# Optimization experiments

Hardware: AMD Instinct MI355X
Metric: run time of the kernel (lower is better)

## Reference

```python
import jax, jax.numpy as jnp
import numpy as np

SLICES = [(12, 1), (13, 1)]  # (input_width, hidden_size=1) per slice


def _lstm_last_hidden(xs, W_ih, W_hh, b):
    """Run a standard (PyTorch gate order i,f,g,o) LSTM over time, return last h.
    xs: [T, B, in]; W_ih: [4*H, in]; W_hh: [4*H, H]; b: [4*H] (b_ih + b_hh).
    Returns h_T: [B, H].
    """
    B = xs.shape[1]
    H = W_hh.shape[1]
    h0 = jnp.zeros((B, H), xs.dtype)
    c0 = jnp.zeros((B, H), xs.dtype)

    def step(carry, xt):
        h, c = carry
        gates = xt @ W_ih.T + h @ W_hh.T + b  # [B, 4H]
        i, f, g, o = jnp.split(gates, 4, axis=-1)
        i = jax.nn.sigmoid(i)
        f = jax.nn.sigmoid(f)
        g = jnp.tanh(g)
        o = jax.nn.sigmoid(o)
        c = f * c + i * g
        h = o * jnp.tanh(c)
        return (h, c), None

    (hT, _), _ = jax.lax.scan(step, (h0, c0), xs)
    return hT


def setup_inputs() -> dict:
    key = jax.random.key(0)
    ks = jax.random.split(key, 9)
    B, T, F = 4096, 512, 25
    nb_out = 1
    s = 0.1
    x = jax.random.normal(ks[0], (B, T, F), dtype=jnp.float32)
    # slice-1 LSTM (input 12, hidden 1)
    W_ih1 = jax.random.normal(ks[1], (4, 12), dtype=jnp.float32) * s
    W_hh1 = jax.random.normal(ks[2], (4, 1), dtype=jnp.float32) * s
    b1 = jax.random.normal(ks[3], (4,), dtype=jnp.float32) * s
    # slice-2 LSTM (input 13, hidden 1)
    W_ih2 = jax.random.normal(ks[4], (4, 13), dtype=jnp.float32) * s
    W_hh2 = jax.random.normal(ks[5], (4, 1), dtype=jnp.float32) * s
    b2 = jax.random.normal(ks[6], (4,), dtype=jnp.float32) * s
    # output head Linear(2, nb_out)
    W_out = jax.random.normal(ks[7], (nb_out, 2), dtype=jnp.float32) * s
    b_out = jax.random.normal(ks[8], (nb_out,), dtype=jnp.float32) * s
    return {"x": x, "W_ih1": W_ih1, "W_hh1": W_hh1, "b1": b1,
            "W_ih2": W_ih2, "W_hh2": W_hh2, "b2": b2,
            "W_out": W_out, "b_out": b_out}


def reference(x, W_ih1, W_hh1, b1, W_ih2, W_hh2, b2, W_out, b_out):
    # x: [B, T, 25] -> time-major [T, B, 25]
    xs = jnp.transpose(x, (1, 0, 2))
    h1 = _lstm_last_hidden(xs[..., :12], W_ih1, W_hh1, b1)   # [B, 1]
    h2 = _lstm_last_hidden(xs[..., 12:], W_ih2, W_hh2, b2)   # [B, 1]
    h = jnp.concatenate([h1, h2], axis=-1)                   # [B, 2] == lstm_out[:, -1, :]
    out = h @ W_out.T + b_out                                # [B, nb_out]
    return jax.nn.sigmoid(out)
```

## Files before the change

### kernel.cpp

```cpp
#include <hip/hip_runtime.h>
#include <stdint.h>


#define T_STEPS 512
#define F_IN    25
#define TC      16
#define NTILES  (T_STEPS / TC)
#define CH      8
#define XROW    520
#define ZROW    (TC * 8 + 8)
#define LOG2E   1.44269504088896340736f

typedef const __attribute__((address_space(1))) void* as1_cvp;
typedef __attribute__((address_space(3)))       void* as3_vp;

__device__ __forceinline__ void gll16(const float* gsrc, const float* ldst) {
  __builtin_amdgcn_global_load_lds((as1_cvp)(uintptr_t)gsrc,
                                   (as3_vp)(uint32_t)(uintptr_t)ldst, 16, 0, 0);
}

__device__ __forceinline__ float sigm(float v) {
  return __builtin_amdgcn_rcpf(1.0f + __builtin_amdgcn_exp2f(v * (-LOG2E)));
}
__device__ __forceinline__ float tanh_(float v) {
  return fmaf(2.0f, __builtin_amdgcn_rcpf(1.0f + __builtin_amdgcn_exp2f(v * (-2.0f * LOG2E))), -1.0f);
}

__device__ __forceinline__ void prefetch_tile(const float* __restrict__ x, int b0, int tile,
                                              float* xbuf, int lane) {
  const float* base = x + (size_t)b0 * (T_STEPS * F_IN) + tile * (TC * F_IN);
  const int i1 = lane * 4;
  int i2 = 256 + lane * 4;
  if (i2 > 396) i2 = 396;
#pragma unroll
  for (int cc = 0; cc < CH; ++cc) {
    const float* g0 = base + cc * (T_STEPS * F_IN);
    gll16(g0 + i1, xbuf + cc * XROW);
    gll16(g0 + i2, xbuf + cc * XROW + 256);
  }
}

__device__ __forceinline__ void gemv_tile(const float* __restrict__ xbuf, float* __restrict__ zbuf,
                                          int c, int lt,
                                          const float* __restrict__ w1, const float* __restrict__ w2,
                                          const float* __restrict__ zb) {
#pragma unroll
  for (int p = 0; p < 2; ++p) {
    const int tl = p * 8 + lt;
    const float* xr = xbuf + c * XROW + tl * F_IN;
    float z[8];
#pragma unroll
    for (int j = 0; j < 8; ++j) z[j] = zb[j];
#pragma unroll
    for (int f = 0; f < 12; ++f) {
      const float xv = xr[f];
#pragma unroll
      for (int j = 0; j < 4; ++j) z[j] = fmaf(w1[j * 12 + f], xv, z[j]);
    }
#pragma unroll
    for (int f = 0; f < 13; ++f) {
      const float xv = xr[12 + f];
#pragma unroll
      for (int j = 0; j < 4; ++j) z[4 + j] = fmaf(w2[j * 13 + f], xv, z[4 + j]);
    }
    float4* zp = (float4*)(zbuf + c * ZROW + tl * 8);
    zp[0] = make_float4(z[0], z[1], z[2], z[3]);
    zp[1] = make_float4(z[4], z[5], z[6], z[7]);
  }
}

__device__ __forceinline__ void scan_tile(const float* __restrict__ zbuf, int c, int zoff,
                                          const float* __restrict__ whh, float& hv, float& cv) {
#pragma unroll
  for (int t = 0; t < TC; ++t) {
    const float4 z4 = *(const float4*)(zbuf + c * ZROW + t * 8 + zoff);
    const float pi = fmaf(hv, whh[0], z4.x);
    const float pf = fmaf(hv, whh[1], z4.y);
    const float pg = fmaf(hv, whh[2], z4.z);
    const float po = fmaf(hv, whh[3], z4.w);
    const float ai = sigm(pi);
    const float af = sigm(pf);
    const float ag = tanh_(pg);
    const float ao = sigm(po);
    cv = fmaf(af, cv, ai * ag);
    hv = ao * tanh_(cv);
  }
}

__global__ void __launch_bounds__(64, 1)
lstm2_fused(const float* __restrict__ x,
            const float* __restrict__ Wih1, const float* __restrict__ Whh1, const float* __restrict__ b1,
            const float* __restrict__ Wih2, const float* __restrict__ Whh2, const float* __restrict__ b2,
            const float* __restrict__ Wout, const float* __restrict__ bout,
            float* __restrict__ out)
{
  __shared__ __align__(16) float xs0[CH * XROW];
  __shared__ __align__(16) float xs1[CH * XROW];
  __shared__ __align__(16) float zs0[CH * ZROW];
  __shared__ __align__(16) float zs1[CH * ZROW];

  const int lane = threadIdx.x;
  const int c    = lane >> 3;
  const int g    = lane & 7;
  const int b0   = blockIdx.x * CH;
  const int zoff = g & 4;

  float w1[48], w2[52], zb[8], whh[4];
#pragma unroll
  for (int j = 0; j < 48; ++j) w1[j] = Wih1[j];
#pragma unroll
  for (int j = 0; j < 52; ++j) w2[j] = Wih2[j];
#pragma unroll
  for (int j = 0; j < 4; ++j) { zb[j] = b1[j]; zb[4 + j] = b2[j]; }
#pragma unroll
  for (int j = 0; j < 4; ++j) whh[j] = (g < 4) ? Whh1[j] : Whh2[j];

  float hv = 0.0f, cv = 0.0f;

  prefetch_tile(x, b0, 0, xs0, lane);
  asm volatile("s_waitcnt vmcnt(0)" ::: "memory");
  prefetch_tile(x, b0, 1, xs1, lane);
  gemv_tile(xs0, zs0, c, g, w1, w2, zb);
  asm volatile("s_waitcnt lgkmcnt(0)" ::: "memory");

  for (int k = 0; k < NTILES - 1; ++k) {
    asm volatile("s_waitcnt vmcnt(0)" ::: "memory");
    int tn = k + 2;
    if (tn > NTILES - 1) tn = NTILES - 1;
    prefetch_tile(x, b0, tn, (k & 1) ? xs1 : xs0, lane);
    const float* zrd = (k & 1) ? zs1 : zs0;
    const float* xrd = (k & 1) ? xs0 : xs1;
    float*       zwr = (k & 1) ? zs0 : zs1;
    scan_tile(zrd, c, zoff, whh, hv, cv);
    gemv_tile(xrd, zwr, c, g, w1, w2, zb);
    asm volatile("s_waitcnt lgkmcnt(0)" ::: "memory");
  }
  scan_tile(zs1, c, zoff, whh, hv, cv);

  const float h1 = __shfl(hv, (lane & 56) + 0, 64);
  const float h2 = __shfl(hv, (lane & 56) + 4, 64);
  if (g == 0) {
    out[b0 + c] = sigm(fmaf(Wout[0], h1, fmaf(Wout[1], h2, bout[0])));
  }
}

extern "C" void kernel_launch(void* const* d_in, const int* in_sizes, int n_in,
                              void* d_out, int out_size, void* d_ws, size_t ws_size,
                              hipStream_t stream) {
  const float* x    = (const float*)d_in[0];
  const float* Wih1 = (const float*)d_in[1];
  const float* Whh1 = (const float*)d_in[2];
  const float* b1   = (const float*)d_in[3];
  const float* Wih2 = (const float*)d_in[4];
  const float* Whh2 = (const float*)d_in[5];
  const float* b2   = (const float*)d_in[6];
  const float* Wout = (const float*)d_in[7];
  const float* bout = (const float*)d_in[8];
  float* out = (float*)d_out;

  const int B = in_sizes[0] / (T_STEPS * F_IN);
  dim3 grid(B / CH), block(64);
  hipLaunchKernelGGL(lstm2_fused, grid, block, 0, stream,
                     x, Wih1, Whh1, b1, Wih2, Whh2, b2, Wout, bout, out);
}
```

Before: 304.5 us.

## Shrink batch per block, split lanes by LSTM half, triple-buffer input tiles

Each block now handles 2 batch rows instead of 8, so four times as many blocks launch. Within a row, 32 lanes split into two halves of 16: one half computes the LSTM1 gate projections and the other LSTM2, one time step per lane. The input prefetch moves from double to triple buffering, with partial vmcnt waits so loads for later tiles stay in flight. The aim is more concurrent waves to hide the latency of the serial recurrence and the global loads; the cost is more redundant scan lanes and more weight registers loaded per block.

After: 309.9 us. About the same (+1.7%).

```diff
diff --git a/kernel.cpp b/kernel.cpp
--- a/kernel.cpp
+++ b/kernel.cpp
@@ -6,9 +6,11 @@
 #define F_IN    25
 #define TC      16
 #define NTILES  (T_STEPS / TC)
-#define CH      8
+#define CH      2
 #define XROW    520
-#define ZROW    (TC * 8 + 8)
+#define ZROW    136
+#define XBUF    (CH * XROW)
+#define ZBUF    (CH * ZROW)
 #define LOG2E   1.44269504088896340736f
 
 typedef const __attribute__((address_space(1))) void* as1_cvp;
@@ -41,32 +43,19 @@
 }
 
 __device__ __forceinline__ void gemv_tile(const float* __restrict__ xbuf, float* __restrict__ zbuf,
-                                          int c, int lt,
-                                          const float* __restrict__ w1, const float* __restrict__ w2,
-                                          const float* __restrict__ zb) {
+                                          int c, int lt, int xoff, int zoff,
+                                          const float* __restrict__ w, const float* __restrict__ zb) {
+  const float* xr = xbuf + c * XROW + lt * F_IN + xoff;
+  float z0 = zb[0], z1 = zb[1], z2 = zb[2], z3 = zb[3];
 #pragma unroll
-  for (int p = 0; p < 2; ++p) {
-    const int tl = p * 8 + lt;
-    const float* xr = xbuf + c * XROW + tl * F_IN;
-    float z[8];
-#pragma unroll
-    for (int j = 0; j < 8; ++j) z[j] = zb[j];
-#pragma unroll
-    for (int f = 0; f < 12; ++f) {
-      const float xv = xr[f];
-#pragma unroll
-      for (int j = 0; j < 4; ++j) z[j] = fmaf(w1[j * 12 + f], xv, z[j]);
-    }
-#pragma unroll
-    for (int f = 0; f < 13; ++f) {
-      const float xv = xr[12 + f];
-#pragma unroll
-      for (int j = 0; j < 4; ++j) z[4 + j] = fmaf(w2[j * 13 + f], xv, z[4 + j]);
-    }
-    float4* zp = (float4*)(zbuf + c * ZROW + tl * 8);
-    zp[0] = make_float4(z[0], z[1], z[2], z[3]);
-    zp[1] = make_float4(z[4], z[5], z[6], z[7]);
+  for (int f = 0; f < 13; ++f) {
+    const float xv = xr[f];
+    z0 = fmaf(w[0 * 13 + f], xv, z0);
+    z1 = fmaf(w[1 * 13 + f], xv, z1);
+    z2 = fmaf(w[2 * 13 + f], xv, z2);
+    z3 = fmaf(w[3 * 13 + f], xv, z3);
   }
+  *(float4*)(zbuf + c * ZROW + lt * 8 + zoff) = make_float4(z0, z1, z2, z3);
 }
 
 __device__ __forceinline__ void scan_tile(const float* __restrict__ zbuf, int c, int zoff,
@@ -87,59 +76,68 @@
   }
 }
 
-__global__ void __launch_bounds__(64, 1)
+__global__ void __launch_bounds__(64, 2)
 lstm2_fused(const float* __restrict__ x,
             const float* __restrict__ Wih1, const float* __restrict__ Whh1, const float* __restrict__ b1,
             const float* __restrict__ Wih2, const float* __restrict__ Whh2, const float* __restrict__ b2,
             const float* __restrict__ Wout, const float* __restrict__ bout,
             float* __restrict__ out)
 {
-  __shared__ __align__(16) float xs0[CH * XROW];
-  __shared__ __align__(16) float xs1[CH * XROW];
-  __shared__ __align__(16) float zs0[CH * ZROW];
-  __shared__ __align__(16) float zs1[CH * ZROW];
+  __shared__ __align__(16) float xs[3 * XBUF];
+  __shared__ __align__(16) float zs[2 * ZBUF];
 
   const int lane = threadIdx.x;
-  const int c    = lane >> 3;
-  const int g    = lane & 7;
+  const int c    = lane >> 5;
+  const int lt   = lane & 15;
+  const int half = (lane >> 4) & 1;
+  const int xoff = half * 12;
+  const int zoff = half * 4;
   const int b0   = blockIdx.x * CH;
-  const int zoff = g & 4;
 
-  float w1[48], w2[52], zb[8], whh[4];
+  float w[52], zb[4], whh[4];
 #pragma unroll
-  for (int j = 0; j < 48; ++j) w1[j] = Wih1[j];
+  for (int j = 0; j < 4; ++j) {
 #pragma unroll
-  for (int j = 0; j < 52; ++j) w2[j] = Wih2[j];
-#pragma unroll
-  for (int j = 0; j < 4; ++j) { zb[j] = b1[j]; zb[4 + j] = b2[j]; }
-#pragma unroll
-  for (int j = 0; j < 4; ++j) whh[j] = (g < 4) ? Whh1[j] : Whh2[j];
+    for (int f = 0; f < 13; ++f) {
+      const float wa = (f < 12) ? Wih1[j * 12 + f] : 0.0f;
+      const float wb = Wih2[j * 13 + f];
+      w[j * 13 + f] = half ? wb : wa;
+    }
+    zb[j]  = half ? b2[j]   : b1[j];
+    whh[j] = half ? Whh2[j] : Whh1[j];
+  }
 
   float hv = 0.0f, cv = 0.0f;
 
-  prefetch_tile(x, b0, 0, xs0, lane);
-  asm volatile("s_waitcnt vmcnt(0)" ::: "memory");
-  prefetch_tile(x, b0, 1, xs1, lane);
-  gemv_tile(xs0, zs0, c, g, w1, w2, zb);
+  prefetch_tile(x, b0, 0, xs + 0 * XBUF, lane);
+  prefetch_tile(x, b0, 1, xs + 1 * XBUF, lane);
+  prefetch_tile(x, b0, 2, xs + 2 * XBUF, lane);
+  asm volatile("s_waitcnt vmcnt(8)" ::: "memory");
+  gemv_tile(xs, zs, c, lt, xoff, zoff, w, zb);
   asm volatile("s_waitcnt lgkmcnt(0)" ::: "memory");
 
+  int pb = 0;
+  int rb = 1;
   for (int k = 0; k < NTILES - 1; ++k) {
-    asm volatile("s_waitcnt vmcnt(0)" ::: "memory");
-    int tn = k + 2;
+    asm volatile("s_waitcnt vmcnt(4)" ::: "memory");
+    int tn = k + 3;
     if (tn > NTILES - 1) tn = NTILES - 1;
-    prefetch_tile(x, b0, tn, (k & 1) ? xs1 : xs0, lane);
-    const float* zrd = (k & 1) ? zs1 : zs0;
-    const float* xrd = (k & 1) ? xs0 : xs1;
-    float*       zwr = (k & 1) ? zs0 : zs1;
+    prefetch_tile(x, b0, tn, xs + pb * XBUF, lane);
+    pb = (pb == 2) ? 0 : pb + 1;
+    const float* zrd = zs + (k & 1) * ZBUF;
+    float*       zwr = zs + ((k + 1) & 1) * ZBUF;
+    const float* xrd = xs + rb * XBUF;
+    rb = (rb == 2) ? 0 : rb + 1;
     scan_tile(zrd, c, zoff, whh, hv, cv);
-    gemv_tile(xrd, zwr, c, g, w1, w2, zb);
+    gemv_tile(xrd, zwr, c, lt, xoff, zoff, w, zb);
     asm volatile("s_waitcnt lgkmcnt(0)" ::: "memory");
   }
-  scan_tile(zs1, c, zoff, whh, hv, cv);
+  scan_tile(zs + ZBUF, c, zoff, whh, hv, cv);
+  asm volatile("s_waitcnt vmcnt(0)" ::: "memory");
 
-  const float h1 = __shfl(hv, (lane & 56) + 0, 64);
-  const float h2 = __shfl(hv, (lane & 56) + 4, 64);
-  if (g == 0) {
+  const float h1 = __shfl(hv, (lane & 32) + 0, 64);
+  const float h2 = __shfl(hv, (lane & 32) + 16, 64);
+  if ((lane & 31) == 0) {
     out[b0 + c] = sigm(fmaf(Wout[0], h1, fmaf(Wout[1], h2, bout[0])));
   }
 }
```
